# Kernel optimization log

Measured on AMD Instinct MI355X. Metric: run time of the kernel, lower is better.

Reference implementation:

```python
import jax, jax.numpy as jnp
import numpy as np

B, S, C = 4, 2048, 1024

def setup_inputs() -> dict:
    key = jax.random.key(0)
    ks = jax.random.split(key, 9)
    lim = 1.0 / np.sqrt(C)  # torch nn.Linear default init range
    def lin_params(kw, kb):
        W = jax.random.uniform(kw, (C, C), jnp.float32, -lim, lim)
        b = jax.random.uniform(kb, (C,), jnp.float32, -lim, lim)
        return W, b
    Wq, bq = lin_params(ks[0], ks[1])
    Wk, bk = lin_params(ks[2], ks[3])
    Wv, bv = lin_params(ks[4], ks[5])
    query = jax.random.normal(ks[6], (B, S, C), jnp.float32)
    key_t = jax.random.normal(ks[7], (B, S, C), jnp.float32)
    value = jax.random.normal(ks[8], (B, S, C), jnp.float32)
    return {"query": query, "key": key_t, "value": value,
            "Wq": Wq, "bq": bq, "Wk": Wk, "bk": bk, "Wv": Wv, "bv": bv}

def reference(query, key, value, Wq, bq, Wk, bk, Wv, bv):
    # Linear projections: y = x @ W^T + b (torch Linear convention, W is [out, in])
    Q = jnp.einsum('bsc,dc->bsd', query, Wq) + bq
    K = jnp.einsum('bsc,dc->bsd', key, Wk) + bk
    V = jnp.einsum('bsc,dc->bsd', value, Wv) + bv
    scale = jnp.float32(C) ** 0.5
    scores = jnp.einsum('bqd,bkd->bqk', Q, K) / scale  # [B, S, S]
    attn = jax.nn.softmax(scores, axis=-1)
    out = jnp.einsum('bqk,bkd->bqd', attn, V)  # [B, S, C]
    return out
```

## Files before the change

### kernel.cpp

```cpp
#include <hip/hip_runtime.h>
#include <hip/hip_bf16.h>


typedef _Float16 half8 __attribute__((ext_vector_type(8)));
typedef _Float16 half4 __attribute__((ext_vector_type(4)));
typedef float f32x4 __attribute__((ext_vector_type(4)));

#define AS1(p) ((const __attribute__((address_space(1))) void*)(p))
#define AS3(p) ((__attribute__((address_space(3))) void*)(p))

__global__ __launch_bounds__(256) void cvt3_f32_f16(
    const float* __restrict__ s0, const float* __restrict__ s1,
    const float* __restrict__ s2, _Float16* __restrict__ d0,
    _Float16* __restrict__ d1, _Float16* __restrict__ d2, int n) {
    const float* s = blockIdx.y == 0 ? s0 : blockIdx.y == 1 ? s1 : s2;
    _Float16* d = blockIdx.y == 0 ? d0 : blockIdx.y == 1 ? d1 : d2;
    int i = (blockIdx.x * 256 + threadIdx.x) * 8;
    if (i >= n) return;
    float4 a = *(const float4*)(s + i);
    float4 b = *(const float4*)(s + i + 4);
    half8 h;
    h[0] = (_Float16)a.x; h[1] = (_Float16)a.y; h[2] = (_Float16)a.z; h[3] = (_Float16)a.w;
    h[4] = (_Float16)b.x; h[5] = (_Float16)b.y; h[6] = (_Float16)b.z; h[7] = (_Float16)b.w;
    *(half8*)(d + i) = h;
}

template <int K, int NX_SH, int R, int NYT_SH, bool BIAS, bool F16OUT, bool PROJ3>
__global__ __launch_bounds__(256, 2)
void gemm_nt(const _Float16* __restrict__ A, const _Float16* __restrict__ Bt,
             const float* __restrict__ b0, const float* __restrict__ b1,
             const float* __restrict__ b2, void* __restrict__ Cout,
             _Float16* __restrict__ VtOut, int N, float scale,
             long sA, long sB, long sC) {
    __shared__ _Float16 Asm[128 * 64] __attribute__((aligned(16)));
    __shared__ _Float16 Bsm[128 * 64] __attribute__((aligned(16)));
    const int tid = threadIdx.x;
    const int lane = tid & 63;
    const int wave = tid >> 6;

    const int lin = blockIdx.x;
    const int g = lin & 7;
    const int s = lin >> 3;
    const int xt = s & ((1 << NX_SH) - 1);
    const int row_id = g * R + (s >> NX_SH);
    const int yt = row_id & ((1 << NYT_SH) - 1);
    const int tz = row_id >> NYT_SH;
    const int m0 = yt * 128;
    const int n0 = xt * 128;

    const float* bias = nullptr;
    if constexpr (PROJ3) {
        A += (long)tz * 8388608;
        Bt += (long)tz * 1048576;
        bias = tz == 0 ? b0 : tz == 1 ? b1 : b2;
    } else {
        A += (long)tz * sA;
        Bt += (long)tz * sB;
    }

    const int srow8 = lane >> 3;
    const int sq = ((lane & 7) ^ srow8) << 3;
    const int quad = lane >> 4;
    const int l16 = lane & 15;
    const int wm = (wave >> 1) << 6;
    const int wn = (wave & 1) << 6;
    const int fa0 = (wm + l16) * 64 + (((0 * 4 + quad) ^ (l16 & 7)) << 3);
    const int fa1 = (wm + l16) * 64 + (((1 * 4 + quad) ^ (l16 & 7)) << 3);
    const int fb0 = (wn + l16) * 64 + (((0 * 4 + quad) ^ (l16 & 7)) << 3);
    const int fb1 = (wn + l16) * 64 + (((1 * 4 + quad) ^ (l16 & 7)) << 3);

    f32x4 acc[4][4];
#pragma unroll
    for (int i = 0; i < 4; i++)
#pragma unroll
        for (int j = 0; j < 4; j++)
#pragma unroll
            for (int r = 0; r < 4; r++) acc[i][j][r] = 0.0f;

    const _Float16* Abase = A + (long)m0 * K;
    const _Float16* Bbase = Bt + (long)n0 * K;

    for (int k0 = 0; k0 < K; k0 += 64) {
        __syncthreads();
#pragma unroll
        for (int u = 0; u < 8; ++u) {
            const int t = wave + u * 4;
            if (t < 16) {
                __builtin_amdgcn_global_load_lds(
                    AS1(Abase + (long)(t * 8 + srow8) * K + k0 + sq),
                    AS3(Asm + t * 512), 16, 0, 0);
            } else {
                __builtin_amdgcn_global_load_lds(
                    AS1(Bbase + (long)((t - 16) * 8 + srow8) * K + k0 + sq),
                    AS3(Bsm + (t - 16) * 512), 16, 0, 0);
            }
        }
        __syncthreads();

#pragma unroll
        for (int ks = 0; ks < 2; ++ks) {
            const int ao = ks ? fa1 : fa0;
            const int bo = ks ? fb1 : fb0;
            half8 af[4], bf[4];
#pragma unroll
            for (int i = 0; i < 4; i++) af[i] = *(const half8*)(Asm + ao + i * 1024);
#pragma unroll
            for (int j = 0; j < 4; j++) bf[j] = *(const half8*)(Bsm + bo + j * 1024);
#pragma unroll
            for (int i = 0; i < 4; i++)
#pragma unroll
                for (int j = 0; j < 4; j++)
                    acc[i][j] = __builtin_amdgcn_mfma_f32_16x16x32_f16(af[i], bf[j], acc[i][j], 0, 0, 0);
        }
    }

    const bool trout = PROJ3 && tz == 2;
#pragma unroll
    for (int i = 0; i < 4; i++) {
        const int row = m0 + wm + i * 16 + quad * 4;
#pragma unroll
        for (int j = 0; j < 4; j++) {
            const int col = n0 + wn + j * 16 + l16;
            const float badd = BIAS ? bias[col] : 0.0f;
            if (trout) {
                const long b = row >> 11;
                const int sl = row & 2047;
                half4 h;
#pragma unroll
                for (int r = 0; r < 4; r++) h[r] = (_Float16)(acc[i][j][r] * scale + badd);
                *(half4*)(VtOut + b * 2097152 + (long)col * 2048 + sl) = h;
            } else if constexpr (PROJ3) {
                _Float16* o = (_Float16*)Cout + (long)tz * 8388608;
#pragma unroll
                for (int r = 0; r < 4; r++)
                    o[(long)(row + r) * N + col] = (_Float16)(acc[i][j][r] * scale + badd);
            } else {
#pragma unroll
                for (int r = 0; r < 4; r++) {
                    float v = acc[i][j][r] * scale + badd;
                    if constexpr (F16OUT)
                        ((_Float16*)Cout + (long)tz * sC)[(long)(row + r) * N + col] = (_Float16)v;
                    else
                        ((float*)Cout + (long)tz * sC)[(long)(row + r) * N + col] = v;
                }
            }
        }
    }
}

__global__ __launch_bounds__(256) void softmax_f16(const _Float16* __restrict__ S,
                                                   _Float16* __restrict__ P) {
    const long row = blockIdx.x;
    const int t = threadIdx.x;
    const int wave = t >> 6, lane = t & 63;
    half8 h = ((const half8*)(S + row * 2048))[t];
    float v[8];
#pragma unroll
    for (int j = 0; j < 8; j++) v[j] = (float)h[j];
    float m = v[0];
#pragma unroll
    for (int j = 1; j < 8; j++) m = fmaxf(m, v[j]);
#pragma unroll
    for (int off = 32; off > 0; off >>= 1) m = fmaxf(m, __shfl_xor(m, off, 64));
    __shared__ float redm[4], reds[4];
    if (lane == 0) redm[wave] = m;
    __syncthreads();
    m = fmaxf(fmaxf(redm[0], redm[1]), fmaxf(redm[2], redm[3]));
    float sum = 0.0f;
#pragma unroll
    for (int j = 0; j < 8; j++) { v[j] = __expf(v[j] - m); sum += v[j]; }
#pragma unroll
    for (int off = 32; off > 0; off >>= 1) sum += __shfl_xor(sum, off, 64);
    if (lane == 0) reds[wave] = sum;
    __syncthreads();
    sum = (reds[0] + reds[1]) + (reds[2] + reds[3]);
    const float inv = 1.0f / sum;
    half8 o;
#pragma unroll
    for (int j = 0; j < 8; j++) o[j] = (_Float16)(v[j] * inv);
    ((half8*)(P + row * 2048))[t] = o;
}

extern "C" void kernel_launch(void* const* d_in, const int* in_sizes, int n_in,
                              void* d_out, int out_size, void* d_ws, size_t ws_size,
                              hipStream_t stream) {
    constexpr int B = 4, S = 2048, C = 1024;
    constexpr long XSZ = (long)B * S * C;
    constexpr long WSZ = (long)C * C;

    const float* query = (const float*)d_in[0];
    const float* key   = (const float*)d_in[1];
    const float* value = (const float*)d_in[2];
    const float* Wq = (const float*)d_in[3];
    const float* bq = (const float*)d_in[4];
    const float* Wk = (const float*)d_in[5];
    const float* bk = (const float*)d_in[6];
    const float* Wv = (const float*)d_in[7];
    const float* bv = (const float*)d_in[8];
    float* out = (float*)d_out;
    char* ws = (char*)d_ws;

    _Float16* Xq  = (_Float16*)(ws + 0);
    _Float16* Wqh = (_Float16*)(ws + 3 * XSZ * 2);
    _Float16* scores = (_Float16*)(ws + 0);
    _Float16* Qh  = (_Float16*)(ws + 73400320);
    _Float16* attn = (_Float16*)(ws + 73400320);
    _Float16* Vt  = (_Float16*)(ws + 106954752);
    if (ws_size < 123731968) return;

    cvt3_f32_f16<<<dim3(XSZ / 2048, 3), 256, 0, stream>>>(
        query, key, value, Xq, Xq + XSZ, Xq + 2 * XSZ, (int)XSZ);
    cvt3_f32_f16<<<dim3(WSZ / 2048, 3), 256, 0, stream>>>(
        Wq, Wk, Wv, Wqh, Wqh + WSZ, Wqh + 2 * WSZ, (int)WSZ);

    gemm_nt<1024, 3, 24, 6, true, true, true><<<1536, 256, 0, stream>>>(
        Xq, Wqh, bq, bk, bv, Qh, Vt, C, 1.0f, 0, 0, 0);

    gemm_nt<1024, 4, 8, 4, false, true, false><<<1024, 256, 0, stream>>>(
        Qh, Qh + XSZ, nullptr, nullptr, nullptr, scores, nullptr, S, 0.03125f,
        (long)S * C, (long)S * C, (long)S * S);

    softmax_f16<<<B * S, 256, 0, stream>>>(scores, attn);

    gemm_nt<2048, 3, 8, 4, false, false, false><<<512, 256, 0, stream>>>(
        attn, Vt, nullptr, nullptr, nullptr, out, nullptr, C, 1.0f,
        (long)S * S, (long)C * S, (long)S * C);
}
```

Measured before the change: 308.2 us.

## Switch GEMMs to single-wave 64x64 tiles with double-buffered LDS and no barriers

Rewrites the GEMM kernel so each block is one 64-lane wave computing a 64x64 tile with k-steps of 32. It ping-pongs two LDS buffers, issuing the next global_load_lds before computing on the current one. Because a block is a single wave, the __syncthreads calls are removed. The trade-offs are 4x more blocks, less data reuse per tile (more global/L2 traffic), and reliance on implicit wave ordering for LDS hazards, with no explicit vmcnt wait shown, which may be a correctness risk.

```diff
diff --git a/kernel.cpp b/kernel.cpp
--- a/kernel.cpp
+++ b/kernel.cpp
@@ -25,31 +25,31 @@
     *(half8*)(d + i) = h;
 }
 
-template <int K, int NX_SH, int R, int NYT_SH, bool BIAS, bool F16OUT, bool PROJ3>
-__global__ __launch_bounds__(256, 2)
+template <int K, int NX_SH, int RR, int NYT_SH, int MODE>
+__global__ __launch_bounds__(64, 2)
 void gemm_nt(const _Float16* __restrict__ A, const _Float16* __restrict__ Bt,
              const float* __restrict__ b0, const float* __restrict__ b1,
              const float* __restrict__ b2, void* __restrict__ Cout,
              _Float16* __restrict__ VtOut, int N, float scale,
              long sA, long sB, long sC) {
-    __shared__ _Float16 Asm[128 * 64] __attribute__((aligned(16)));
-    __shared__ _Float16 Bsm[128 * 64] __attribute__((aligned(16)));
-    const int tid = threadIdx.x;
-    const int lane = tid & 63;
-    const int wave = tid >> 6;
+    __shared__ _Float16 A0[2048] __attribute__((aligned(16)));
+    __shared__ _Float16 B0[2048] __attribute__((aligned(16)));
+    __shared__ _Float16 A1[2048] __attribute__((aligned(16)));
+    __shared__ _Float16 B1[2048] __attribute__((aligned(16)));
+    const int l = threadIdx.x;
 
     const int lin = blockIdx.x;
     const int g = lin & 7;
     const int s = lin >> 3;
     const int xt = s & ((1 << NX_SH) - 1);
-    const int row_id = g * R + (s >> NX_SH);
+    const int row_id = g * RR + (s >> NX_SH);
     const int yt = row_id & ((1 << NYT_SH) - 1);
     const int tz = row_id >> NYT_SH;
-    const int m0 = yt * 128;
-    const int n0 = xt * 128;
+    const int m0 = yt * 64;
+    const int n0 = xt * 64;
 
     const float* bias = nullptr;
-    if constexpr (PROJ3) {
+    if constexpr (MODE == 0) {
         A += (long)tz * 8388608;
         Bt += (long)tz * 1048576;
         bias = tz == 0 ? b0 : tz == 1 ? b1 : b2;
@@ -58,16 +58,14 @@
         Bt += (long)tz * sB;
     }
 
-    const int srow8 = lane >> 3;
-    const int sq = ((lane & 7) ^ srow8) << 3;
-    const int quad = lane >> 4;
-    const int l16 = lane & 15;
-    const int wm = (wave >> 1) << 6;
-    const int wn = (wave & 1) << 6;
-    const int fa0 = (wm + l16) * 64 + (((0 * 4 + quad) ^ (l16 & 7)) << 3);
-    const int fa1 = (wm + l16) * 64 + (((1 * 4 + quad) ^ (l16 & 7)) << 3);
-    const int fb0 = (wn + l16) * 64 + (((0 * 4 + quad) ^ (l16 & 7)) << 3);
-    const int fb1 = (wn + l16) * 64 + (((1 * 4 + quad) ^ (l16 & 7)) << 3);
+    const int larow = l >> 2;
+    const int lchunk = (((l & 3) ^ ((l >> 3) & 3)) << 3);
+    const int quad = l >> 4;
+    const int l16 = l & 15;
+    const int rdoff = ((quad ^ ((l16 >> 1) & 3)) << 3);
+
+    const _Float16* Ag = A + (long)m0 * K;
+    const _Float16* Bg = Bt + (long)n0 * K;
 
     f32x4 acc[4][4];
 #pragma unroll
@@ -77,72 +75,73 @@
 #pragma unroll
             for (int r = 0; r < 4; r++) acc[i][j][r] = 0.0f;
 
-    const _Float16* Abase = A + (long)m0 * K;
-    const _Float16* Bbase = Bt + (long)n0 * K;
-
+#define STAGE(Ad, Bd, k0)                                                        \
+    {                                                                            \
+        _Pragma("unroll") for (int u = 0; u < 4; ++u) {                          \
+            __builtin_amdgcn_global_load_lds(                                    \
+                AS1(Ag + (long)(u * 16 + larow) * K + (k0) + lchunk),            \
+                AS3(Ad + u * 512), 16, 0, 0);                                    \
+            __builtin_amdgcn_global_load_lds(                                    \
+                AS1(Bg + (long)(u * 16 + larow) * K + (k0) + lchunk),            \
+                AS3(Bd + u * 512), 16, 0, 0);                                    \
+        }                                                                        \
+    }
+
+#define COMPUTE(As, Bs)                                                          \
+    {                                                                            \
+        half8 af[4], bf[4];                                                      \
+        _Pragma("unroll") for (int i = 0; i < 4; i++)                            \
+            af[i] = *(const half8*)(As + (i * 16 + l16) * 32 + rdoff);           \
+        _Pragma("unroll") for (int j = 0; j < 4; j++)                            \
+            bf[j] = *(const half8*)(Bs + (j * 16 + l16) * 32 + rdoff);           \
+        _Pragma("unroll") for (int i = 0; i < 4; i++)                            \
+            _Pragma("unroll") for (int j = 0; j < 4; j++)                        \
+                acc[i][j] =                                                      \
+                    __builtin_amdgcn_mfma_f32_16x16x32_f16(af[i], bf[j],         \
+                                                           acc[i][j], 0, 0, 0); \
+    }
+
+    STAGE(A0, B0, 0)
     for (int k0 = 0; k0 < K; k0 += 64) {
-        __syncthreads();
-#pragma unroll
-        for (int u = 0; u < 8; ++u) {
-            const int t = wave + u * 4;
-            if (t < 16) {
-                __builtin_amdgcn_global_load_lds(
-                    AS1(Abase + (long)(t * 8 + srow8) * K + k0 + sq),
-                    AS3(Asm + t * 512), 16, 0, 0);
+        STAGE(A1, B1, k0 + 32)
+        COMPUTE(A0, B0)
+        if (k0 + 64 < K) STAGE(A0, B0, k0 + 64)
+        COMPUTE(A1, B1)
+    }
+#undef STAGE
+#undef COMPUTE
+
+#pragma unroll
+    for (int i = 0; i < 4; i++) {
+        const int row = m0 + i * 16 + quad * 4;
+#pragma unroll
+        for (int j = 0; j < 4; j++) {
+            const int col = n0 + j * 16 + l16;
+            if constexpr (MODE == 0) {
+                const float badd = bias[col];
+                if (tz == 2) {
+                    const long b = row >> 11;
+                    const int sl = row & 2047;
+                    half4 h;
+#pragma unroll
+                    for (int r = 0; r < 4; r++) h[r] = (_Float16)(acc[i][j][r] + badd);
+                    *(half4*)(VtOut + b * 2097152 + (long)col * 2048 + sl) = h;
+                } else {
+                    _Float16* o = (_Float16*)Cout + (long)tz * 8388608;
+#pragma unroll
+                    for (int r = 0; r < 4; r++)
+                        o[(long)(row + r) * N + col] = (_Float16)(acc[i][j][r] + badd);
+                }
+            } else if constexpr (MODE == 1) {
+#pragma unroll
+                for (int r = 0; r < 4; r++)
+                    ((_Float16*)Cout + (long)tz * sC)[(long)(row + r) * N + col] =
+                        (_Float16)(acc[i][j][r] * scale);
             } else {
-                __builtin_amdgcn_global_load_lds(
-                    AS1(Bbase + (long)((t - 16) * 8 + srow8) * K + k0 + sq),
-                    AS3(Bsm + (t - 16) * 512), 16, 0, 0);
-            }
-        }
-        __syncthreads();
-
-#pragma unroll
-        for (int ks = 0; ks < 2; ++ks) {
-            const int ao = ks ? fa1 : fa0;
-            const int bo = ks ? fb1 : fb0;
-            half8 af[4], bf[4];
-#pragma unroll
-            for (int i = 0; i < 4; i++) af[i] = *(const half8*)(Asm + ao + i * 1024);
-#pragma unroll
-            for (int j = 0; j < 4; j++) bf[j] = *(const half8*)(Bsm + bo + j * 1024);
-#pragma unroll
-            for (int i = 0; i < 4; i++)
-#pragma unroll
-                for (int j = 0; j < 4; j++)
-                    acc[i][j] = __builtin_amdgcn_mfma_f32_16x16x32_f16(af[i], bf[j], acc[i][j], 0, 0, 0);
-        }
-    }
-
-    const bool trout = PROJ3 && tz == 2;
-#pragma unroll
-    for (int i = 0; i < 4; i++) {
-        const int row = m0 + wm + i * 16 + quad * 4;
-#pragma unroll
-        for (int j = 0; j < 4; j++) {
-            const int col = n0 + wn + j * 16 + l16;
-            const float badd = BIAS ? bias[col] : 0.0f;
-            if (trout) {
-                const long b = row >> 11;
-                const int sl = row & 2047;
-                half4 h;
-#pragma unroll
-                for (int r = 0; r < 4; r++) h[r] = (_Float16)(acc[i][j][r] * scale + badd);
-                *(half4*)(VtOut + b * 2097152 + (long)col * 2048 + sl) = h;
-            } else if constexpr (PROJ3) {
-                _Float16* o = (_Float16*)Cout + (long)tz * 8388608;
 #pragma unroll
                 for (int r = 0; r < 4; r++)
-                    o[(long)(row + r) * N + col] = (_Float16)(acc[i][j][r] * scale + badd);
-            } else {
-#pragma unroll
-                for (int r = 0; r < 4; r++) {
-                    float v = acc[i][j][r] * scale + badd;
-                    if constexpr (F16OUT)
-                        ((_Float16*)Cout + (long)tz * sC)[(long)(row + r) * N + col] = (_Float16)v;
-                    else
-                        ((float*)Cout + (long)tz * sC)[(long)(row + r) * N + col] = v;
-                }
+                    ((float*)Cout + (long)tz * sC)[(long)(row + r) * N + col] =
+                        acc[i][j][r];
             }
         }
     }
@@ -213,16 +212,16 @@
     cvt3_f32_f16<<<dim3(WSZ / 2048, 3), 256, 0, stream>>>(
         Wq, Wk, Wv, Wqh, Wqh + WSZ, Wqh + 2 * WSZ, (int)WSZ);
 
-    gemm_nt<1024, 3, 24, 6, true, true, true><<<1536, 256, 0, stream>>>(
+    gemm_nt<1024, 4, 48, 7, 0><<<6144, 64, 0, stream>>>(
         Xq, Wqh, bq, bk, bv, Qh, Vt, C, 1.0f, 0, 0, 0);
 
-    gemm_nt<1024, 4, 8, 4, false, true, false><<<1024, 256, 0, stream>>>(
+    gemm_nt<1024, 5, 16, 5, 1><<<4096, 64, 0, stream>>>(
         Qh, Qh + XSZ, nullptr, nullptr, nullptr, scores, nullptr, S, 0.03125f,
         (long)S * C, (long)S * C, (long)S * S);
 
     softmax_f16<<<B * S, 256, 0, stream>>>(scores, attn);
 
-    gemm_nt<2048, 3, 8, 4, false, false, false><<<512, 256, 0, stream>>>(
+    gemm_nt<2048, 4, 16, 5, 2><<<2048, 64, 0, stream>>>(
         attn, Vt, nullptr, nullptr, nullptr, out, nullptr, C, 1.0f,
         (long)S * S, (long)C * S, (long)S * C);
 }
```

Measured after the change: 409.9 us. 1.33x slower.

## Load A fragments directly from global memory and merge conversion kernels

Applied to the files above, without the earlier changes.

The GEMM stops staging the A tile in shared memory. Each wave now reads its A fragments straight from global memory into registers, and only B goes through LDS. This halves LDS use and the async-copy traffic, which may allow higher occupancy. The cost is uncoalesced 16-byte global loads of A whose latency is not hidden by any prefetch, and the two waves sharing A rows load it redundantly. Separately, the input and weight conversion launches are merged into one six-slice launch, which wastes many early-exiting blocks on the weight slices.

```diff
diff --git a/kernel.cpp b/kernel.cpp
--- a/kernel.cpp
+++ b/kernel.cpp
@@ -9,13 +9,16 @@
 #define AS1(p) ((const __attribute__((address_space(1))) void*)(p))
 #define AS3(p) ((__attribute__((address_space(3))) void*)(p))
 
-__global__ __launch_bounds__(256) void cvt3_f32_f16(
-    const float* __restrict__ s0, const float* __restrict__ s1,
-    const float* __restrict__ s2, _Float16* __restrict__ d0,
-    _Float16* __restrict__ d1, _Float16* __restrict__ d2, int n) {
-    const float* s = blockIdx.y == 0 ? s0 : blockIdx.y == 1 ? s1 : s2;
-    _Float16* d = blockIdx.y == 0 ? d0 : blockIdx.y == 1 ? d1 : d2;
-    int i = (blockIdx.x * 256 + threadIdx.x) * 8;
+__global__ __launch_bounds__(256) void cvt6_f32_f16(
+    const float* __restrict__ i0, const float* __restrict__ i1,
+    const float* __restrict__ i2, const float* __restrict__ w0,
+    const float* __restrict__ w1, const float* __restrict__ w2,
+    _Float16* __restrict__ di, _Float16* __restrict__ dw, long n0, long n1) {
+    const int y = blockIdx.y;
+    const float* s; _Float16* d; long n;
+    if (y < 3) { s = y == 0 ? i0 : y == 1 ? i1 : i2; d = di + (long)y * n0; n = n0; }
+    else       { s = y == 3 ? w0 : y == 4 ? w1 : w2; d = dw + (long)(y - 3) * n1; n = n1; }
+    long i = ((long)blockIdx.x * 256 + threadIdx.x) * 8;
     if (i >= n) return;
     float4 a = *(const float4*)(s + i);
     float4 b = *(const float4*)(s + i + 4);
@@ -32,7 +35,6 @@
              const float* __restrict__ b2, void* __restrict__ Cout,
              _Float16* __restrict__ VtOut, int N, float scale,
              long sA, long sB, long sC) {
-    __shared__ _Float16 Asm[128 * 64] __attribute__((aligned(16)));
     __shared__ _Float16 Bsm[128 * 64] __attribute__((aligned(16)));
     const int tid = threadIdx.x;
     const int lane = tid & 63;
@@ -64,10 +66,8 @@
     const int l16 = lane & 15;
     const int wm = (wave >> 1) << 6;
     const int wn = (wave & 1) << 6;
-    const int fa0 = (wm + l16) * 64 + (((0 * 4 + quad) ^ (l16 & 7)) << 3);
-    const int fa1 = (wm + l16) * 64 + (((1 * 4 + quad) ^ (l16 & 7)) << 3);
-    const int fb0 = (wn + l16) * 64 + (((0 * 4 + quad) ^ (l16 & 7)) << 3);
-    const int fb1 = (wn + l16) * 64 + (((1 * 4 + quad) ^ (l16 & 7)) << 3);
+    const int fb0 = (wn + l16) * 64 + ((quad ^ (l16 & 7)) << 3);
+    const int fb1 = (wn + l16) * 64 + (((4 + quad) ^ (l16 & 7)) << 3);
 
     f32x4 acc[4][4];
 #pragma unroll
@@ -77,33 +77,27 @@
 #pragma unroll
             for (int r = 0; r < 4; r++) acc[i][j][r] = 0.0f;
 
-    const _Float16* Abase = A + (long)m0 * K;
+    const _Float16* Afrag = A + (long)(m0 + wm + l16) * K + quad * 8;
     const _Float16* Bbase = Bt + (long)n0 * K;
 
     for (int k0 = 0; k0 < K; k0 += 64) {
         __syncthreads();
 #pragma unroll
-        for (int u = 0; u < 8; ++u) {
+        for (int u = 0; u < 4; ++u) {
             const int t = wave + u * 4;
-            if (t < 16) {
-                __builtin_amdgcn_global_load_lds(
-                    AS1(Abase + (long)(t * 8 + srow8) * K + k0 + sq),
-                    AS3(Asm + t * 512), 16, 0, 0);
-            } else {
-                __builtin_amdgcn_global_load_lds(
-                    AS1(Bbase + (long)((t - 16) * 8 + srow8) * K + k0 + sq),
-                    AS3(Bsm + (t - 16) * 512), 16, 0, 0);
-            }
+            __builtin_amdgcn_global_load_lds(
+                AS1(Bbase + (long)(t * 8 + srow8) * K + k0 + sq),
+                AS3(Bsm + t * 512), 16, 0, 0);
         }
         __syncthreads();
 
 #pragma unroll
         for (int ks = 0; ks < 2; ++ks) {
-            const int ao = ks ? fa1 : fa0;
             const int bo = ks ? fb1 : fb0;
             half8 af[4], bf[4];
 #pragma unroll
-            for (int i = 0; i < 4; i++) af[i] = *(const half8*)(Asm + ao + i * 1024);
+            for (int i = 0; i < 4; i++)
+                af[i] = *(const half8*)(Afrag + (long)i * 16 * K + k0 + ks * 32);
 #pragma unroll
             for (int j = 0; j < 4; j++) bf[j] = *(const half8*)(Bsm + bo + j * 1024);
 #pragma unroll
@@ -208,10 +202,8 @@
     _Float16* Vt  = (_Float16*)(ws + 106954752);
     if (ws_size < 123731968) return;
 
-    cvt3_f32_f16<<<dim3(XSZ / 2048, 3), 256, 0, stream>>>(
-        query, key, value, Xq, Xq + XSZ, Xq + 2 * XSZ, (int)XSZ);
-    cvt3_f32_f16<<<dim3(WSZ / 2048, 3), 256, 0, stream>>>(
-        Wq, Wk, Wv, Wqh, Wqh + WSZ, Wqh + 2 * WSZ, (int)WSZ);
+    cvt6_f32_f16<<<dim3(XSZ / 2048, 6), 256, 0, stream>>>(
+        query, key, value, Wq, Wk, Wv, Xq, Wqh, XSZ, WSZ);
 
     gemm_nt<1024, 3, 24, 6, true, true, true><<<1536, 256, 0, stream>>>(
         Xq, Wqh, bq, bk, bv, Qh, Vt, C, 1.0f, 0, 0, 0);
```

New measurement: 459.7 us. +49.2%, slower.
